# Performance work log

Measured on AMD Instinct MI355X. Metric: run time of the kernel, lower is better.

## Reference

```python
import jax, jax.numpy as jnp
import numpy as np

BN_EPS = 1e-5


def _square_distance(src, dst):
    # src: (B,N,3), dst: (B,S,3) -> (B,N,S) squared euclidean distance
    d = -2.0 * jnp.einsum('bnc,bsc->bns', src, dst)
    d += jnp.sum(src * src, -1)[:, :, None]
    d += jnp.sum(dst * dst, -1)[:, None, :]
    return d


def _bn_relu(x, gamma, beta):
    # training-mode BatchNorm1d over (B, C, N): stats over (B, N)
    mean = jnp.mean(x, axis=(0, 2), keepdims=True)
    var = jnp.var(x, axis=(0, 2), keepdims=True)  # biased, as torch uses for normalization
    xhat = (x - mean) * jax.lax.rsqrt(var + BN_EPS)
    return jax.nn.relu(xhat * gamma[None, :, None] + beta[None, :, None])


def setup_inputs() -> dict:
    key = jax.random.key(0)
    ks = jax.random.split(key, 8)
    B, N, S, C1, C2 = 4, 8192, 2048, 128, 256
    inp = {
        'xyz1': jax.random.normal(ks[0], (B, 3, N), jnp.float32),
        'xyz2': jax.random.normal(ks[1], (B, 3, S), jnp.float32),
        'points1': jax.random.normal(ks[2], (B, C1, N), jnp.float32),
        'points2': jax.random.normal(ks[3], (B, C2, S), jnp.float32),
        'w0': jax.random.normal(ks[4], (256, C1 + C2), jnp.float32) * (1.0 / np.sqrt(C1 + C2)),
        'b0': jnp.zeros((256,), jnp.float32),
        'gamma0': jnp.ones((256,), jnp.float32),
        'beta0': jnp.zeros((256,), jnp.float32),
        'w1': jax.random.normal(ks[5], (128, 256), jnp.float32) * (1.0 / np.sqrt(256)),
        'b1': jnp.zeros((128,), jnp.float32),
        'gamma1': jnp.ones((128,), jnp.float32),
        'beta1': jnp.zeros((128,), jnp.float32),
    }
    return inp


def reference(xyz1, xyz2, points1, points2, w0, b0, gamma0, beta0, w1, b1, gamma1, beta1):
    B, _, N = xyz1.shape
    S = xyz2.shape[2]
    xyz1_t = jnp.transpose(xyz1, (0, 2, 1))  # (B,N,3)
    xyz2_t = jnp.transpose(xyz2, (0, 2, 1))  # (B,S,3)
    dist = _square_distance(xyz1_t, xyz2_t)  # (B,N,S)
    neg_d3, idx = jax.lax.top_k(-dist, 3)    # 3 smallest distances
    d3 = -neg_d3                             # (B,N,3)
    dist_recip = 1.0 / (d3 + 1e-8)
    weight = dist_recip / jnp.sum(dist_recip, axis=2, keepdims=True)  # (B,N,3)
    points2_t = jnp.transpose(points2, (0, 2, 1))  # (B,S,C2)
    bidx = jnp.arange(B)[:, None, None]
    neighbor = points2_t[bidx, idx]                 # (B,N,3,C2)
    interp = jnp.sum(neighbor * weight[..., None], axis=2)  # (B,N,C2)
    interp = jnp.transpose(interp, (0, 2, 1))               # (B,C2,N)
    x = jnp.concatenate([points1, interp], axis=1)          # (B,C1+C2,N)
    x = _bn_relu(jnp.einsum('oc,bcn->bon', w0, x) + b0[None, :, None], gamma0, beta0)
    x = _bn_relu(jnp.einsum('oc,bcn->bon', w1, x) + b1[None, :, None], gamma1, beta1)
    return x
```

## Files before the change

### kernel.cpp

```cpp
#include <hip/hip_runtime.h>
#include <hip/hip_bf16.h>

#define BATCH 4
#define NPTS  8192
#define SPTS  2048
#define C1    128
#define C2    256
#define CIN   384
#define H0    256
#define H1    128

typedef __attribute__((ext_vector_type(8))) short bf16x8;
typedef __attribute__((ext_vector_type(4))) float f32x4;

__device__ __forceinline__ unsigned short f2bf(float x) {
  union { float f; unsigned u; } v; v.f = x;
  unsigned r = v.u + 0x7fff + ((v.u >> 16) & 1);
  return (unsigned short)(r >> 16);
}
__device__ __forceinline__ float bf2f(unsigned short u) {
  union { unsigned u; float f; } v; v.u = ((unsigned)u) << 16; return v.f;
}

__global__ __launch_bounds__(256) void transpose_p2_kernel(
    const float* __restrict__ p2, float* __restrict__ p2t) {
  __shared__ float tile[64][65];
  int b = blockIdx.z;
  int s0 = blockIdx.x * 64, c0 = blockIdx.y * 64;
  const float* src = p2 + (size_t)b * C2 * SPTS;
  float* dst = p2t + (size_t)b * SPTS * C2;
  int t = threadIdx.x;
  int ss = t & 63, cseg = t >> 6;
#pragma unroll
  for (int i = 0; i < 16; i++) {
    int cc = cseg + i * 4;
    tile[cc][ss] = src[(size_t)(c0 + cc) * SPTS + s0 + ss];
  }
  __syncthreads();
  int cc2 = t & 63, sseg = t >> 6;
#pragma unroll
  for (int i = 0; i < 16; i++) {
    int ss2 = sseg + i * 4;
    dst[(size_t)(s0 + ss2) * C2 + c0 + cc2] = tile[cc2][ss2];
  }
}

__global__ __launch_bounds__(256) void prepack_xyz2_kernel(
    const float* __restrict__ xyz2, float4* __restrict__ xp) {
  int idx = blockIdx.x * 256 + threadIdx.x;
  int b = idx >> 11;
  int s = idx & (SPTS - 1);
  const float* x2 = xyz2 + (size_t)b * 3 * SPTS;
  float x = x2[s], y = x2[SPTS + s], z = x2[2 * SPTS + s];
  xp[idx] = make_float4(x, y, z, x * x + y * y + z * z);
}

__global__ __launch_bounds__(512) void knn_kernel(
    const float* __restrict__ xyz1, const float4* __restrict__ xp,
    int* __restrict__ nidx, float* __restrict__ nw) {
  int b = blockIdx.y;
  int t = threadIdx.x;
  int lane = t & 63;
  int chunk = __builtin_amdgcn_readfirstlane(t >> 6);
  int n = blockIdx.x * 64 + lane;
  const float* x1 = xyz1 + (size_t)b * 3 * NPTS;
  float px = x1[n], py = x1[NPTS + n], pz = x1[2 * NPTS + n];

  const int CHUNK = SPTS / 8;
  int sbase = chunk * CHUNK;
  const float4* cp = xp + (size_t)b * SPTS + sbase;

  float d0 = 3e38f, d1 = 3e38f, d2 = 3e38f;
  int i0 = 0, i1 = 0, i2 = 0;
#pragma unroll 4
  for (int j = 0; j < CHUNK; j++) {
    float4 c = cp[j];
    float qc = px * c.x;
    qc = fmaf(py, c.y, qc);
    qc = fmaf(pz, c.z, qc);
    float d = fmaf(-2.f, qc, c.w);
    int s = sbase + j;
    bool lt0 = d < d0, lt1 = d < d1, lt2 = d < d2;
    i2 = lt1 ? i1 : (lt2 ? s : i2);
    d2 = lt1 ? d1 : (lt2 ? d : d2);
    i1 = lt0 ? i0 : (lt1 ? s : i1);
    d1 = lt0 ? d0 : (lt1 ? d : d1);
    i0 = lt0 ? s : i0;
    d0 = lt0 ? d : d0;
  }

  __shared__ float dsh[8][64][3];
  __shared__ int   ish[8][64][3];
  dsh[chunk][lane][0] = d0; dsh[chunk][lane][1] = d1; dsh[chunk][lane][2] = d2;
  ish[chunk][lane][0] = i0; ish[chunk][lane][1] = i1; ish[chunk][lane][2] = i2;
  __syncthreads();

  if (t < 64) {
    float e0 = 3e38f, e1 = 3e38f, e2 = 3e38f;
    int j0 = 0, j1 = 0, j2 = 0;
#pragma unroll
    for (int c = 0; c < 8; c++) {
#pragma unroll
      for (int k = 0; k < 3; k++) {
        float d = dsh[c][t][k];
        int s = ish[c][t][k];
        bool lt0 = d < e0, lt1 = d < e1, lt2 = d < e2;
        j2 = lt1 ? j1 : (lt2 ? s : j2);
        e2 = lt1 ? e1 : (lt2 ? d : e2);
        j1 = lt0 ? j0 : (lt1 ? s : j1);
        e1 = lt0 ? e0 : (lt1 ? d : e1);
        j0 = lt0 ? s : j0;
        e0 = lt0 ? d : e0;
      }
    }
    float qq = px * px + py * py + pz * pz;
    float r0 = 1.f / (e0 + qq + 1e-8f);
    float r1 = 1.f / (e1 + qq + 1e-8f);
    float r2 = 1.f / (e2 + qq + 1e-8f);
    float rs = 1.f / (r0 + r1 + r2);
    int base = (b * NPTS + n) * 3;
    nidx[base + 0] = j0; nidx[base + 1] = j1; nidx[base + 2] = j2;
    nw[base + 0] = r0 * rs; nw[base + 1] = r1 * rs; nw[base + 2] = r2 * rs;
  }
}

__global__ __launch_bounds__(256) void pack_p1_kernel(
    const float* __restrict__ p1, unsigned short* __restrict__ Xp) {
  __shared__ unsigned short tile[64][136];
  int b = blockIdx.y, n0 = blockIdx.x * 64;
  int t = threadIdx.x;
  int nn = t & 63, c4 = t >> 6;
#pragma unroll
  for (int i = 0; i < 32; i++) {
    int c = i * 4 + c4;
    tile[nn][c] = f2bf(p1[((size_t)b * C1 + c) * NPTS + n0 + nn]);
  }
  __syncthreads();
  int n = t >> 2;
#pragma unroll
  for (int j = 0; j < 4; j++) {
    int ch = (t & 3) + j * 4;
    uint4 v = *(const uint4*)&tile[n][ch * 8];
    *(uint4*)&Xp[((size_t)b * NPTS + n0 + n) * CIN + ch * 8] = v;
  }
}

__global__ __launch_bounds__(256) void interp_kernel(
    const float* __restrict__ p2t, const int* __restrict__ nidx,
    const float* __restrict__ nw, unsigned short* __restrict__ Xp) {
  const int PTS = 8;
  int bid = blockIdx.x;
  int b = bid / (NPTS / PTS);
  int p0 = (bid % (NPTS / PTS)) * PTS;
  int c = threadIdx.x;
  const float* base = p2t + (size_t)b * SPTS * C2;
#pragma unroll
  for (int k = 0; k < PTS; k++) {
    int p = p0 + k;
    int ib = (b * NPTS + p) * 3;
    int i0 = nidx[ib], i1 = nidx[ib + 1], i2 = nidx[ib + 2];
    float w0v = nw[ib], w1v = nw[ib + 1], w2v = nw[ib + 2];
    float v = w0v * base[(size_t)i0 * C2 + c] +
              w1v * base[(size_t)i1 * C2 + c] +
              w2v * base[(size_t)i2 * C2 + c];
    Xp[((size_t)b * NPTS + p) * CIN + C1 + c] = f2bf(v);
  }
}

__global__ __launch_bounds__(256) void pack_w_kernel(
    const float* __restrict__ w0, const float* __restrict__ w1,
    unsigned short* __restrict__ Wp) {
  int idx = (blockIdx.x * 256 + threadIdx.x) * 4;
  const float* src = (idx < H0 * CIN) ? (w0 + idx) : (w1 + (idx - H0 * CIN));
  float4 v = *(const float4*)src;
  ushort4 o;
  o.x = f2bf(v.x); o.y = f2bf(v.y); o.z = f2bf(v.z); o.w = f2bf(v.w);
  *(ushort4*)(Wp + idx) = o;
}

template <int MT, int KD, bool OUT_BF16>
__global__ __launch_bounds__(256) void mfma_gemm_kernel(
    const unsigned short* __restrict__ A, const unsigned short* __restrict__ X,
    const float* __restrict__ bias, void* __restrict__ Yv) {
  __shared__ unsigned short As[128 * 32];
  __shared__ unsigned short Bs[128 * 32];
  int b = blockIdx.z;
  int n0 = blockIdx.x * 128;
  int o0 = blockIdx.y * 128;
  int t = threadIdx.x;
  int lane = t & 63;
  int w = __builtin_amdgcn_readfirstlane(t >> 6);
  int mhalf = (w & 1) * 64, nhalf = (w >> 1) * 64;
  const unsigned short* Xb = X + (size_t)b * NPTS * KD;

  f32x4 acc[4][4] = {};

  int rA = lane >> 2;
  int cofs = (lane & 3) * 8;

  for (int k0 = 0; k0 < KD; k0 += 32) {
#pragma unroll
    for (int q = 0; q < 2; q++) {
      int r0 = w * 32 + q * 16;
      const unsigned short* ga = A + (size_t)(o0 + r0 + rA) * KD + k0 + cofs;
      __builtin_amdgcn_global_load_lds(
          (const __attribute__((address_space(1))) void*)ga,
          (__attribute__((address_space(3))) void*)(As + r0 * 32), 16, 0, 0);
      const unsigned short* gb = Xb + (size_t)(n0 + r0 + rA) * KD + k0 + cofs;
      __builtin_amdgcn_global_load_lds(
          (const __attribute__((address_space(1))) void*)gb,
          (__attribute__((address_space(3))) void*)(Bs + r0 * 32), 16, 0, 0);
    }
    __syncthreads();

    bf16x8 af[4], bfr[4];
    int mi = lane & 15, kq = (lane >> 4) * 8;
#pragma unroll
    for (int i = 0; i < 4; i++) {
      af[i]  = *(const bf16x8*)(As + (mhalf + i * 16 + mi) * 32 + kq);
      bfr[i] = *(const bf16x8*)(Bs + (nhalf + i * 16 + mi) * 32 + kq);
    }
#pragma unroll
    for (int mt = 0; mt < 4; mt++)
#pragma unroll
      for (int nt = 0; nt < 4; nt++)
        acc[mt][nt] = __builtin_amdgcn_mfma_f32_16x16x32_bf16(
            af[mt], bfr[nt], acc[mt][nt], 0, 0, 0);
    __syncthreads();
  }

  int mi = lane & 15;
  int rq = (lane >> 4) * 4;
#pragma unroll
  for (int mt = 0; mt < 4; mt++) {
#pragma unroll
    for (int r = 0; r < 4; r++) {
      int m = o0 + mhalf + mt * 16 + rq + r;
      float bv = bias[m];
#pragma unroll
      for (int nt = 0; nt < 4; nt++) {
        int n = n0 + nhalf + nt * 16 + mi;
        float v = acc[mt][nt][r] + bv;
        if constexpr (OUT_BF16) {
          unsigned short* Y = (unsigned short*)Yv + (size_t)b * MT * NPTS;
          Y[(size_t)m * NPTS + n] = f2bf(v);
        } else {
          float* Y = (float*)Yv + (size_t)b * MT * NPTS;
          Y[(size_t)m * NPTS + n] = v;
        }
      }
    }
  }
}

template <int C>
__global__ __launch_bounds__(256) void bn_stats_bf16_kernel(
    const unsigned short* __restrict__ Y, const float* __restrict__ gamma,
    const float* __restrict__ beta, float* __restrict__ a, float* __restrict__ s) {
  int o = blockIdx.x;
  int t = threadIdx.x;
  float sum = 0.f, sq = 0.f;
  for (int b = 0; b < BATCH; b++) {
    const unsigned short* p = Y + ((size_t)b * C + o) * NPTS;
    for (int n = t * 4; n < NPTS; n += 1024) {
      ushort4 v = *(const ushort4*)(p + n);
      float x0 = bf2f(v.x), x1 = bf2f(v.y), x2 = bf2f(v.z), x3 = bf2f(v.w);
      sum += x0 + x1 + x2 + x3;
      sq += x0 * x0 + x1 * x1 + x2 * x2 + x3 * x3;
    }
  }
  __shared__ float r1[256], r2[256];
  r1[t] = sum; r2[t] = sq;
  __syncthreads();
  for (int off = 128; off > 0; off >>= 1) {
    if (t < off) { r1[t] += r1[t + off]; r2[t] += r2[t + off]; }
    __syncthreads();
  }
  if (t == 0) {
    float inv = 1.f / (float)(BATCH * NPTS);
    float mean = r1[0] * inv;
    float var = r2[0] * inv - mean * mean;
    float ia = gamma[o] * rsqrtf(var + 1e-5f);
    a[o] = ia;
    s[o] = beta[o] - mean * ia;
  }
}

template <int C>
__global__ __launch_bounds__(256) void bn_stats_kernel(
    const float* __restrict__ Y, const float* __restrict__ gamma,
    const float* __restrict__ beta, float* __restrict__ a, float* __restrict__ s) {
  int o = blockIdx.x;
  int t = threadIdx.x;
  float sum = 0.f, sq = 0.f;
  for (int b = 0; b < BATCH; b++) {
    const float* p = Y + ((size_t)b * C + o) * NPTS;
    for (int n = t * 4; n < NPTS; n += 1024) {
      float4 v = *(const float4*)(p + n);
      sum += v.x + v.y + v.z + v.w;
      sq += v.x * v.x + v.y * v.y + v.z * v.z + v.w * v.w;
    }
  }
  __shared__ float r1[256], r2[256];
  r1[t] = sum; r2[t] = sq;
  __syncthreads();
  for (int off = 128; off > 0; off >>= 1) {
    if (t < off) { r1[t] += r1[t + off]; r2[t] += r2[t + off]; }
    __syncthreads();
  }
  if (t == 0) {
    float inv = 1.f / (float)(BATCH * NPTS);
    float mean = r1[0] * inv;
    float var = r2[0] * inv - mean * mean;
    float ia = gamma[o] * rsqrtf(var + 1e-5f);
    a[o] = ia;
    s[o] = beta[o] - mean * ia;
  }
}

__global__ __launch_bounds__(256) void bn0_apply_kernel(
    const unsigned short* __restrict__ Y0, const float* __restrict__ a,
    const float* __restrict__ s, unsigned short* __restrict__ X1) {
  __shared__ unsigned short tile[64][80];
  int b = blockIdx.z, o0 = blockIdx.y * 64, n0 = blockIdx.x * 64;
  int t = threadIdx.x;
  int nn = t & 63, o4 = t >> 6;
#pragma unroll
  for (int i = 0; i < 16; i++) {
    int o = i * 4 + o4;
    float v = bf2f(Y0[((size_t)b * H0 + o0 + o) * NPTS + n0 + nn]);
    v = fmaxf(v * a[o0 + o] + s[o0 + o], 0.f);
    tile[nn][o] = f2bf(v);
  }
  __syncthreads();
  int n = t >> 2;
#pragma unroll
  for (int j = 0; j < 2; j++) {
    int ch = (t & 3) + j * 4;
    uint4 v = *(const uint4*)&tile[n][ch * 8];
    *(uint4*)&X1[((size_t)b * NPTS + n0 + n) * H0 + o0 + ch * 8] = v;
  }
}

__global__ __launch_bounds__(256) void bn_apply_kernel(
    float* __restrict__ Y, const float* __restrict__ a, const float* __restrict__ s) {
  int idx = blockIdx.x * 256 + threadIdx.x;
  int i = idx * 4;
  int c = (i >> 13) & (H1 - 1);
  float ia = a[c], sh = s[c];
  float4 v = *(float4*)(Y + i);
  v.x = fmaxf(v.x * ia + sh, 0.f);
  v.y = fmaxf(v.y * ia + sh, 0.f);
  v.z = fmaxf(v.z * ia + sh, 0.f);
  v.w = fmaxf(v.w * ia + sh, 0.f);
  *(float4*)(Y + i) = v;
}

extern "C" void kernel_launch(void* const* d_in, const int* in_sizes, int n_in,
                              void* d_out, int out_size, void* d_ws, size_t ws_size,
                              hipStream_t stream) {
  const float* xyz1    = (const float*)d_in[0];
  const float* xyz2    = (const float*)d_in[1];
  const float* points1 = (const float*)d_in[2];
  const float* points2 = (const float*)d_in[3];
  const float* w0      = (const float*)d_in[4];
  const float* b0      = (const float*)d_in[5];
  const float* gamma0  = (const float*)d_in[6];
  const float* beta0   = (const float*)d_in[7];
  const float* w1      = (const float*)d_in[8];
  const float* b1      = (const float*)d_in[9];
  const float* gamma1  = (const float*)d_in[10];
  const float* beta1   = (const float*)d_in[11];
  float* out = (float*)d_out;

  char* ws = (char*)d_ws;
  float* p2t = (float*)ws;                    ws += (size_t)BATCH * SPTS * C2 * 4;
  unsigned short* Xp = (unsigned short*)ws;   ws += (size_t)BATCH * NPTS * CIN * 2;
  unsigned short* Y0 = (unsigned short*)ws;   ws += (size_t)BATCH * H0 * NPTS * 2;
  unsigned short* X1 = (unsigned short*)ws;   ws += (size_t)BATCH * NPTS * H0 * 2;
  unsigned short* Wp = (unsigned short*)ws;   ws += (size_t)(H0 * CIN + H1 * H0) * 2;
  int* nidx = (int*)ws;                       ws += (size_t)BATCH * NPTS * 3 * 4;
  float* nw = (float*)ws;                     ws += (size_t)BATCH * NPTS * 3 * 4;
  float4* xyz2p = (float4*)ws;                ws += (size_t)BATCH * SPTS * 16;
  float* a0 = (float*)ws;                     ws += 1024;
  float* s0 = (float*)ws;                     ws += 1024;
  float* a1 = (float*)ws;                     ws += 1024;
  float* s1 = (float*)ws;                     ws += 1024;
  (void)ws_size; (void)in_sizes; (void)n_in; (void)out_size;

  transpose_p2_kernel<<<dim3(SPTS / 64, C2 / 64, BATCH), 256, 0, stream>>>(points2, p2t);
  prepack_xyz2_kernel<<<dim3(BATCH * SPTS / 256), 256, 0, stream>>>(xyz2, xyz2p);
  knn_kernel<<<dim3(NPTS / 64, BATCH), 512, 0, stream>>>(xyz1, xyz2p, nidx, nw);
  pack_p1_kernel<<<dim3(NPTS / 64, BATCH), 256, 0, stream>>>(points1, Xp);
  interp_kernel<<<dim3(BATCH * NPTS / 8), 256, 0, stream>>>(p2t, nidx, nw, Xp);
  pack_w_kernel<<<dim3((H0 * CIN + H1 * H0) / 1024), 256, 0, stream>>>(w0, w1, Wp);

  mfma_gemm_kernel<H0, CIN, true><<<dim3(NPTS / 128, H0 / 128, BATCH), 256, 0, stream>>>(
      Wp, Xp, b0, Y0);
  bn_stats_bf16_kernel<H0><<<H0, 256, 0, stream>>>(Y0, gamma0, beta0, a0, s0);
  bn0_apply_kernel<<<dim3(NPTS / 64, H0 / 64, BATCH), 256, 0, stream>>>(Y0, a0, s0, X1);
  mfma_gemm_kernel<H1, H0, false><<<dim3(NPTS / 128, H1 / 128, BATCH), 256, 0, stream>>>(
      Wp + H0 * CIN, X1, b1, out);
  bn_stats_kernel<H1><<<H1, 256, 0, stream>>>(out, gamma1, beta1, a1, s1);
  bn_apply_kernel<<<dim3(BATCH * H1 * NPTS / 1024), 256, 0, stream>>>(out, a1, s1);
}
```

Before: 217.5 us.

## Fuse prep kernels, store points2 transpose in bf16, widen KNN to 16 waves

Merges the points2 transpose, points1 pack, xyz2 prepack and weight pack into one multi-role launch, which cuts launch count and per-launch overhead. The transposed points2 is now stored as bf16, halving the memory traffic of the transpose write and the interpolation gathers at a small precision cost. The KNN kernel splits the candidate set across 16 waves instead of 8, merges partial top-3 lists in two levels, and uses med3/min for the distance insert to shorten the select chain. The larger 1024-thread blocks may reduce occupancy flexibility.

```diff
diff --git a/kernel.cpp b/kernel.cpp
--- a/kernel.cpp
+++ b/kernel.cpp
@@ -22,95 +22,138 @@
   union { unsigned u; float f; } v; v.u = ((unsigned)u) << 16; return v.f;
 }
 
-__global__ __launch_bounds__(256) void transpose_p2_kernel(
-    const float* __restrict__ p2, float* __restrict__ p2t) {
-  __shared__ float tile[64][65];
-  int b = blockIdx.z;
-  int s0 = blockIdx.x * 64, c0 = blockIdx.y * 64;
-  const float* src = p2 + (size_t)b * C2 * SPTS;
-  float* dst = p2t + (size_t)b * SPTS * C2;
-  int t = threadIdx.x;
-  int ss = t & 63, cseg = t >> 6;
-#pragma unroll
-  for (int i = 0; i < 16; i++) {
-    int cc = cseg + i * 4;
-    tile[cc][ss] = src[(size_t)(c0 + cc) * SPTS + s0 + ss];
-  }
-  __syncthreads();
-  int cc2 = t & 63, sseg = t >> 6;
-#pragma unroll
-  for (int i = 0; i < 16; i++) {
-    int ss2 = sseg + i * 4;
-    dst[(size_t)(s0 + ss2) * C2 + c0 + cc2] = tile[cc2][ss2];
-  }
-}
-
-__global__ __launch_bounds__(256) void prepack_xyz2_kernel(
-    const float* __restrict__ xyz2, float4* __restrict__ xp) {
-  int idx = blockIdx.x * 256 + threadIdx.x;
-  int b = idx >> 11;
-  int s = idx & (SPTS - 1);
-  const float* x2 = xyz2 + (size_t)b * 3 * SPTS;
-  float x = x2[s], y = x2[SPTS + s], z = x2[2 * SPTS + s];
-  xp[idx] = make_float4(x, y, z, x * x + y * y + z * z);
-}
-
-__global__ __launch_bounds__(512) void knn_kernel(
+__global__ __launch_bounds__(256) void prep_kernel(
+    const float* __restrict__ p2, unsigned short* __restrict__ p2tb,
+    const float* __restrict__ xyz2, float4* __restrict__ xp,
+    const float* __restrict__ w0, const float* __restrict__ w1,
+    unsigned short* __restrict__ Wp,
+    const float* __restrict__ p1, unsigned short* __restrict__ Xp) {
+  __shared__ unsigned short shmem[64 * 136];
+  int bid = blockIdx.x;
+  int t = threadIdx.x;
+
+  if (bid < 512) {
+    int b = bid >> 7, rem = bid & 127;
+    int s0 = (rem >> 2) * 64, c0 = (rem & 3) * 64;
+    const float* src = p2 + (size_t)b * C2 * SPTS;
+    int ss = t & 63, cseg = t >> 6;
+#pragma unroll
+    for (int i = 0; i < 16; i++) {
+      int cc = cseg + i * 4;
+      shmem[ss * 72 + cc] = f2bf(src[(size_t)(c0 + cc) * SPTS + s0 + ss]);
+    }
+    __syncthreads();
+    int s = t >> 2, chunk = t & 3;
+    uint4 v0 = *(const uint4*)&shmem[s * 72 + chunk * 16];
+    uint4 v1 = *(const uint4*)&shmem[s * 72 + chunk * 16 + 8];
+    unsigned short* dst = p2tb + (size_t)b * SPTS * C2 + (size_t)(s0 + s) * C2 + c0 + chunk * 16;
+    *(uint4*)dst = v0;
+    *(uint4*)(dst + 8) = v1;
+  } else if (bid < 1024) {
+    int b2 = bid - 512;
+    int b = b2 >> 7, n0 = (b2 & 127) * 64;
+    int nn = t & 63, c4 = t >> 6;
+#pragma unroll
+    for (int i = 0; i < 32; i++) {
+      int c = i * 4 + c4;
+      shmem[nn * 136 + c] = f2bf(p1[((size_t)b * C1 + c) * NPTS + n0 + nn]);
+    }
+    __syncthreads();
+    int n = t >> 2;
+#pragma unroll
+    for (int j = 0; j < 4; j++) {
+      int ch = (t & 3) + j * 4;
+      uint4 v = *(const uint4*)&shmem[n * 136 + ch * 8];
+      *(uint4*)&Xp[((size_t)b * NPTS + n0 + n) * CIN + ch * 8] = v;
+    }
+  } else if (bid < 1056) {
+    int idx = (bid - 1024) * 256 + t;
+    int b = idx >> 11, s = idx & (SPTS - 1);
+    const float* x2 = xyz2 + (size_t)b * 3 * SPTS;
+    float x = x2[s], y = x2[SPTS + s], z = x2[2 * SPTS + s];
+    xp[idx] = make_float4(x, y, z, x * x + y * y + z * z);
+  } else {
+    int idx = ((bid - 1056) * 256 + t) * 4;
+    const float* src = (idx < H0 * CIN) ? (w0 + idx) : (w1 + (idx - H0 * CIN));
+    float4 v = *(const float4*)src;
+    ushort4 o;
+    o.x = f2bf(v.x); o.y = f2bf(v.y); o.z = f2bf(v.z); o.w = f2bf(v.w);
+    *(ushort4*)(Wp + idx) = o;
+  }
+}
+
+#define INS3(d, s, e0, e1, e2, j0, j1, j2)                        \
+  {                                                               \
+    bool lt0 = (d) < (e0), lt1 = (d) < (e1), lt2 = (d) < (e2);    \
+    j2 = lt1 ? (j1) : (lt2 ? (s) : (j2));                         \
+    j1 = lt0 ? (j0) : (lt1 ? (s) : (j1));                         \
+    j0 = lt0 ? (s) : (j0);                                        \
+    e2 = __builtin_amdgcn_fmed3f((d), (e1), (e2));                \
+    e1 = __builtin_amdgcn_fmed3f((d), (e0), (e1));                \
+    e0 = fminf((d), (e0));                                        \
+  }
+
+__global__ __launch_bounds__(1024) void knn_kernel(
     const float* __restrict__ xyz1, const float4* __restrict__ xp,
     int* __restrict__ nidx, float* __restrict__ nw) {
   int b = blockIdx.y;
   int t = threadIdx.x;
   int lane = t & 63;
-  int chunk = __builtin_amdgcn_readfirstlane(t >> 6);
+  int w = __builtin_amdgcn_readfirstlane(t >> 6);
   int n = blockIdx.x * 64 + lane;
   const float* x1 = xyz1 + (size_t)b * 3 * NPTS;
   float px = x1[n], py = x1[NPTS + n], pz = x1[2 * NPTS + n];
 
-  const int CHUNK = SPTS / 8;
-  int sbase = chunk * CHUNK;
+  const int CHUNK = SPTS / 16;
+  int sbase = w * CHUNK;
   const float4* cp = xp + (size_t)b * SPTS + sbase;
 
   float d0 = 3e38f, d1 = 3e38f, d2 = 3e38f;
   int i0 = 0, i1 = 0, i2 = 0;
-#pragma unroll 4
+#pragma unroll 8
   for (int j = 0; j < CHUNK; j++) {
     float4 c = cp[j];
-    float qc = px * c.x;
-    qc = fmaf(py, c.y, qc);
+    float qc = fmaf(py, c.y, px * c.x);
     qc = fmaf(pz, c.z, qc);
     float d = fmaf(-2.f, qc, c.w);
     int s = sbase + j;
-    bool lt0 = d < d0, lt1 = d < d1, lt2 = d < d2;
-    i2 = lt1 ? i1 : (lt2 ? s : i2);
-    d2 = lt1 ? d1 : (lt2 ? d : d2);
-    i1 = lt0 ? i0 : (lt1 ? s : i1);
-    d1 = lt0 ? d0 : (lt1 ? d : d1);
-    i0 = lt0 ? s : i0;
-    d0 = lt0 ? d : d0;
-  }
-
-  __shared__ float dsh[8][64][3];
-  __shared__ int   ish[8][64][3];
-  dsh[chunk][lane][0] = d0; dsh[chunk][lane][1] = d1; dsh[chunk][lane][2] = d2;
-  ish[chunk][lane][0] = i0; ish[chunk][lane][1] = i1; ish[chunk][lane][2] = i2;
+    INS3(d, s, d0, d1, d2, i0, i1, i2);
+  }
+
+  __shared__ float dsh[16][64][3];
+  __shared__ int   ish[16][64][3];
+  dsh[w][lane][0] = d0; dsh[w][lane][1] = d1; dsh[w][lane][2] = d2;
+  ish[w][lane][0] = i0; ish[w][lane][1] = i1; ish[w][lane][2] = i2;
+  __syncthreads();
+
+  if (t < 256) {
+    int g = t >> 6, q = t & 63;
+    float e0 = 3e38f, e1 = 3e38f, e2 = 3e38f;
+    int j0 = 0, j1 = 0, j2 = 0;
+#pragma unroll
+    for (int c = 0; c < 4; c++) {
+#pragma unroll
+      for (int k = 0; k < 3; k++) {
+        float d = dsh[4 * g + c][q][k];
+        int s = ish[4 * g + c][q][k];
+        INS3(d, s, e0, e1, e2, j0, j1, j2);
+      }
+    }
+    dsh[4 * g][q][0] = e0; dsh[4 * g][q][1] = e1; dsh[4 * g][q][2] = e2;
+    ish[4 * g][q][0] = j0; ish[4 * g][q][1] = j1; ish[4 * g][q][2] = j2;
+  }
   __syncthreads();
 
   if (t < 64) {
     float e0 = 3e38f, e1 = 3e38f, e2 = 3e38f;
     int j0 = 0, j1 = 0, j2 = 0;
 #pragma unroll
-    for (int c = 0; c < 8; c++) {
+    for (int c = 0; c < 4; c++) {
 #pragma unroll
       for (int k = 0; k < 3; k++) {
-        float d = dsh[c][t][k];
-        int s = ish[c][t][k];
-        bool lt0 = d < e0, lt1 = d < e1, lt2 = d < e2;
-        j2 = lt1 ? j1 : (lt2 ? s : j2);
-        e2 = lt1 ? e1 : (lt2 ? d : e2);
-        j1 = lt0 ? j0 : (lt1 ? s : j1);
-        e1 = lt0 ? e0 : (lt1 ? d : e1);
-        j0 = lt0 ? s : j0;
-        e0 = lt0 ? d : e0;
+        float d = dsh[4 * c][t][k];
+        int s = ish[4 * c][t][k];
+        INS3(d, s, e0, e1, e2, j0, j1, j2);
       }
     }
     float qq = px * px + py * py + pz * pz;
@@ -124,58 +167,26 @@
   }
 }
 
-__global__ __launch_bounds__(256) void pack_p1_kernel(
-    const float* __restrict__ p1, unsigned short* __restrict__ Xp) {
-  __shared__ unsigned short tile[64][136];
-  int b = blockIdx.y, n0 = blockIdx.x * 64;
-  int t = threadIdx.x;
-  int nn = t & 63, c4 = t >> 6;
-#pragma unroll
-  for (int i = 0; i < 32; i++) {
-    int c = i * 4 + c4;
-    tile[nn][c] = f2bf(p1[((size_t)b * C1 + c) * NPTS + n0 + nn]);
-  }
-  __syncthreads();
-  int n = t >> 2;
-#pragma unroll
-  for (int j = 0; j < 4; j++) {
-    int ch = (t & 3) + j * 4;
-    uint4 v = *(const uint4*)&tile[n][ch * 8];
-    *(uint4*)&Xp[((size_t)b * NPTS + n0 + n) * CIN + ch * 8] = v;
-  }
-}
-
 __global__ __launch_bounds__(256) void interp_kernel(
-    const float* __restrict__ p2t, const int* __restrict__ nidx,
+    const unsigned short* __restrict__ p2tb, const int* __restrict__ nidx,
     const float* __restrict__ nw, unsigned short* __restrict__ Xp) {
   const int PTS = 8;
   int bid = blockIdx.x;
   int b = bid / (NPTS / PTS);
   int p0 = (bid % (NPTS / PTS)) * PTS;
   int c = threadIdx.x;
-  const float* base = p2t + (size_t)b * SPTS * C2;
+  const unsigned short* base = p2tb + (size_t)b * SPTS * C2;
 #pragma unroll
   for (int k = 0; k < PTS; k++) {
     int p = p0 + k;
     int ib = (b * NPTS + p) * 3;
     int i0 = nidx[ib], i1 = nidx[ib + 1], i2 = nidx[ib + 2];
     float w0v = nw[ib], w1v = nw[ib + 1], w2v = nw[ib + 2];
-    float v = w0v * base[(size_t)i0 * C2 + c] +
-              w1v * base[(size_t)i1 * C2 + c] +
-              w2v * base[(size_t)i2 * C2 + c];
+    float v = w0v * bf2f(base[(size_t)i0 * C2 + c]) +
+              w1v * bf2f(base[(size_t)i1 * C2 + c]) +
+              w2v * bf2f(base[(size_t)i2 * C2 + c]);
     Xp[((size_t)b * NPTS + p) * CIN + C1 + c] = f2bf(v);
   }
-}
-
-__global__ __launch_bounds__(256) void pack_w_kernel(
-    const float* __restrict__ w0, const float* __restrict__ w1,
-    unsigned short* __restrict__ Wp) {
-  int idx = (blockIdx.x * 256 + threadIdx.x) * 4;
-  const float* src = (idx < H0 * CIN) ? (w0 + idx) : (w1 + (idx - H0 * CIN));
-  float4 v = *(const float4*)src;
-  ushort4 o;
-  o.x = f2bf(v.x); o.y = f2bf(v.y); o.z = f2bf(v.z); o.w = f2bf(v.w);
-  *(ushort4*)(Wp + idx) = o;
 }
 
 template <int MT, int KD, bool OUT_BF16>
@@ -374,26 +385,25 @@
   float* out = (float*)d_out;
 
   char* ws = (char*)d_ws;
-  float* p2t = (float*)ws;                    ws += (size_t)BATCH * SPTS * C2 * 4;
-  unsigned short* Xp = (unsigned short*)ws;   ws += (size_t)BATCH * NPTS * CIN * 2;
-  unsigned short* Y0 = (unsigned short*)ws;   ws += (size_t)BATCH * H0 * NPTS * 2;
-  unsigned short* X1 = (unsigned short*)ws;   ws += (size_t)BATCH * NPTS * H0 * 2;
-  unsigned short* Wp = (unsigned short*)ws;   ws += (size_t)(H0 * CIN + H1 * H0) * 2;
-  int* nidx = (int*)ws;                       ws += (size_t)BATCH * NPTS * 3 * 4;
-  float* nw = (float*)ws;                     ws += (size_t)BATCH * NPTS * 3 * 4;
-  float4* xyz2p = (float4*)ws;                ws += (size_t)BATCH * SPTS * 16;
-  float* a0 = (float*)ws;                     ws += 1024;
-  float* s0 = (float*)ws;                     ws += 1024;
-  float* a1 = (float*)ws;                     ws += 1024;
-  float* s1 = (float*)ws;                     ws += 1024;
+  unsigned short* p2tb = (unsigned short*)ws;  ws += (size_t)BATCH * SPTS * C2 * 2;
+  unsigned short* Xp = (unsigned short*)ws;    ws += (size_t)BATCH * NPTS * CIN * 2;
+  unsigned short* Y0 = (unsigned short*)ws;    ws += (size_t)BATCH * H0 * NPTS * 2;
+  unsigned short* X1 = (unsigned short*)ws;    ws += (size_t)BATCH * NPTS * H0 * 2;
+  unsigned short* Wp = (unsigned short*)ws;    ws += (size_t)(H0 * CIN + H1 * H0) * 2;
+  int* nidx = (int*)ws;                        ws += (size_t)BATCH * NPTS * 3 * 4;
+  float* nw = (float*)ws;                      ws += (size_t)BATCH * NPTS * 3 * 4;
+  float4* xyz2p = (float4*)(((uintptr_t)ws + 15) & ~(uintptr_t)15);
+  ws = (char*)xyz2p + (size_t)BATCH * SPTS * 16;
+  float* a0 = (float*)ws;                      ws += 1024;
+  float* s0 = (float*)ws;                      ws += 1024;
+  float* a1 = (float*)ws;                      ws += 1024;
+  float* s1 = (float*)ws;                      ws += 1024;
   (void)ws_size; (void)in_sizes; (void)n_in; (void)out_size;
 
-  transpose_p2_kernel<<<dim3(SPTS / 64, C2 / 64, BATCH), 256, 0, stream>>>(points2, p2t);
-  prepack_xyz2_kernel<<<dim3(BATCH * SPTS / 256), 256, 0, stream>>>(xyz2, xyz2p);
-  knn_kernel<<<dim3(NPTS / 64, BATCH), 512, 0, stream>>>(xyz1, xyz2p, nidx, nw);
-  pack_p1_kernel<<<dim3(NPTS / 64, BATCH), 256, 0, stream>>>(points1, Xp);
-  interp_kernel<<<dim3(BATCH * NPTS / 8), 256, 0, stream>>>(p2t, nidx, nw, Xp);
-  pack_w_kernel<<<dim3((H0 * CIN + H1 * H0) / 1024), 256, 0, stream>>>(w0, w1, Wp);
+  prep_kernel<<<dim3(1184), 256, 0, stream>>>(points2, p2tb, xyz2, xyz2p,
+                                              w0, w1, Wp, points1, Xp);
+  knn_kernel<<<dim3(NPTS / 64, BATCH), 1024, 0, stream>>>(xyz1, xyz2p, nidx, nw);
+  interp_kernel<<<dim3(BATCH * NPTS / 8), 256, 0, stream>>>(p2tb, nidx, nw, Xp);
 
   mfma_gemm_kernel<H0, CIN, true><<<dim3(NPTS / 128, H0 / 128, BATCH), 256, 0, stream>>>(
       Wp, Xp, b0, Y0);
```

After: 197.4 us. 9.2% less time.
